# Optimization experiments

Hardware: AMD Instinct MI355X
Metric: run time of the kernel (lower is better)

Reference implementation:

```python
import jax, jax.numpy as jnp
import numpy as np

T, B = 128, 256          # frames, batch (free dims)
C_IN = 201               # in_features
KD = 3                   # keypoint_dimensionality
NK = C_IN // KD          # 67 keypoints = attention seq len
E = 8                    # d_pose_embed
H = 2                    # heads
DH = E // H              # head dim = 4
L = 12                   # encoder layers
FF = 2 * E               # 16
OUT = 128                # output_size
EPS = 1e-5


def setup_inputs() -> dict:
    key = jax.random.key(0)
    ks = jax.random.split(key, 12)
    s = 0.1
    return {
        "pose_clip": jax.random.normal(ks[0], (T, B, C_IN), jnp.float32),
        "embed_w": jax.random.normal(ks[1], (E, KD), jnp.float32) * s,
        "embed_b": jax.random.normal(ks[2], (E,), jnp.float32) * s,
        "in_proj_w": jax.random.normal(ks[3], (L, 3 * E, E), jnp.float32) * s,
        "in_proj_b": jax.random.normal(ks[4], (L, 3 * E), jnp.float32) * s,
        "attn_out_w": jax.random.normal(ks[5], (L, E, E), jnp.float32) * s,
        "attn_out_b": jax.random.normal(ks[6], (L, E), jnp.float32) * s,
        "ff1_w": jax.random.normal(ks[7], (L, FF, E), jnp.float32) * s,
        "ff1_b": jax.random.normal(ks[8], (L, FF), jnp.float32) * s,
        "ff2_w": jax.random.normal(ks[9], (L, E, FF), jnp.float32) * s,
        "ff2_b": jax.random.normal(ks[10], (L, E), jnp.float32) * s,
        "ln1_g": jnp.ones((L, E), jnp.float32),
        "ln1_b": jnp.zeros((L, E), jnp.float32),
        "ln2_g": jnp.ones((L, E), jnp.float32),
        "ln2_b": jnp.zeros((L, E), jnp.float32),
        "out_w": jax.random.normal(ks[11], (OUT, NK * E), jnp.float32) * s,
        "out_b": jnp.zeros((OUT,), jnp.float32),
    }


def _ln(x, g, b):
    m = jnp.mean(x, axis=-1, keepdims=True)
    v = jnp.mean(jnp.square(x - m), axis=-1, keepdims=True)
    return (x - m) * jax.lax.rsqrt(v + EPS) * g + b


def _encoder(x, layer_params):
    # x: [S, N, E]; post-LN TransformerEncoderLayer, relu activation, no dropout (eval)
    def step(h, p):
        ipw, ipb, aow, aob, f1w, f1b, f2w, f2b, g1, b1, g2, b2 = p
        S, N, _ = h.shape
        qkv = h @ ipw.T + ipb                      # [S, N, 3E]
        q, k, v = jnp.split(qkv, 3, axis=-1)
        q = q.reshape(S, N, H, DH)
        k = k.reshape(S, N, H, DH)
        v = v.reshape(S, N, H, DH)
        scores = jnp.einsum('snhd,tnhd->nhst', q, k) / np.sqrt(DH).astype(h.dtype)
        attn = jax.nn.softmax(scores, axis=-1)
        o = jnp.einsum('nhst,tnhd->snhd', attn, v).reshape(S, N, E)
        o = o @ aow.T + aob
        h = _ln(h + o, g1, b1)
        ff = jax.nn.relu(h @ f1w.T + f1b) @ f2w.T + f2b
        h = _ln(h + ff, g2, b2)
        return h, None
    x, _ = jax.lax.scan(step, x, layer_params)
    return x


def reference(pose_clip, embed_w, embed_b, in_proj_w, in_proj_b, attn_out_w,
              attn_out_b, ff1_w, ff1_b, ff2_w, ff2_b, ln1_g, ln1_b, ln2_g,
              ln2_b, out_w, out_b):
    t, b, c = pose_clip.shape
    nk = c // KD
    # [t,b,c] -> [t*b, nk, 3] -> [nk, t*b, 3]  (seq=keypoints, batch=t*b)
    x = pose_clip.reshape(t * b, nk, KD).transpose(1, 0, 2)
    x = x @ embed_w.T + embed_b                    # [nk, t*b, E]
    layer_params = (in_proj_w, in_proj_b, attn_out_w, attn_out_b,
                    ff1_w, ff1_b, ff2_w, ff2_b, ln1_g, ln1_b, ln2_g, ln2_b)
    x = _encoder(x, layer_params)
    x = x.transpose(1, 0, 2).reshape(t, b, nk * E)  # [t, b, 536]
    return jnp.tanh(x @ out_w.T + out_b)            # [t, b, 128]
```

## Files before the change

kernel.cpp:

```cpp
#include <hip/hip_runtime.h>
#include <math.h>

#define NTOT 32768
#define CIN  201
#define S    67
#define E    8
#define H    2
#define L    12
#define FF   16
#define OUTC 128
#define KF   536
#define EPB  7
#define LPE  34
#define THREADS 256
#define NPAIR 34

typedef float v2f __attribute__((ext_vector_type(2)));

#if __has_builtin(__builtin_amdgcn_exp2f)
#define EXP2F(x) __builtin_amdgcn_exp2f(x)
#else
#define EXP2F(x) exp2f(x)
#endif
#if __has_builtin(__builtin_amdgcn_rcpf)
#define RCPF(x) __builtin_amdgcn_rcpf(x)
#else
#define RCPF(x) (1.0f/(x))
#endif
#if __has_builtin(__builtin_amdgcn_rsqf)
#define RSQF(x) __builtin_amdgcn_rsqf(x)
#else
#define RSQF(x) rsqrtf(x)
#endif

#define QSCALE 0.7213475204444817f

__device__ __forceinline__ v2f sp(float x) { return (v2f){x, x}; }

__device__ __forceinline__ void ln8p(v2f* x, const float* __restrict__ gg,
                                     const float* __restrict__ bb) {
    v2f m = {0.f, 0.f};
    #pragma unroll
    for (int e = 0; e < E; ++e) m += x[e];
    m *= 0.125f;
    v2f v = {0.f, 0.f};
    #pragma unroll
    for (int e = 0; e < E; ++e) { v2f d = x[e] - m; v += d * d; }
    v *= 0.125f;
    v2f rs;
    rs.x = RSQF(v.x + 1e-5f);
    rs.y = RSQF(v.y + 1e-5f);
    #pragma unroll
    for (int e = 0; e < E; ++e) x[e] = (x[e] - m) * rs * sp(gg[e]) + sp(bb[e]);
}

__global__ __launch_bounds__(THREADS, 5)
void enc_kernel(const float* __restrict__ pose,
                const float* __restrict__ ew,  const float* __restrict__ ebias,
                const float* __restrict__ ipw, const float* __restrict__ ipb,
                const float* __restrict__ aow, const float* __restrict__ aob,
                const float* __restrict__ f1w, const float* __restrict__ f1b,
                const float* __restrict__ f2w, const float* __restrict__ f2b,
                const float* __restrict__ g1,  const float* __restrict__ b1,
                const float* __restrict__ g2,  const float* __restrict__ b2,
                float* __restrict__ xf)
{
    __shared__ float4 KA[EPB * H][NPAIR];
    __shared__ float4 KB[EPB * H][NPAIR];
    __shared__ float4 VA[EPB * H][NPAIR];
    __shared__ float4 VB[EPB * H][NPAIR];

    const int lid = threadIdx.x;
    const int g   = lid / LPE;
    const int j   = lid - g * LPE;
    const int n   = blockIdx.x * EPB + g;
    const bool active = (g < EPB) && (n < NTOT);
    const bool pad = (j == LPE - 1);
    const int r0 = 2 * j;

    v2f xr[E];
    if (active) {
        const float* p0 = pose + (size_t)n * CIN + 3 * r0;
        const float* p1 = pad ? p0 : (p0 + 3);
        v2f c0 = {p0[0], p1[0]};
        v2f c1 = {p0[1], p1[1]};
        v2f c2 = {p0[2], p1[2]};
        #pragma unroll
        for (int e = 0; e < E; ++e)
            xr[e] = sp(ebias[e]) + c0 * sp(ew[e*3+0]) + c1 * sp(ew[e*3+1])
                                 + c2 * sp(ew[e*3+2]);
    }

    #pragma unroll 1
    for (int l = 0; l < L; ++l) {
        const float* W  = ipw + l * 192;
        const float* Bq = ipb + l * 24;

        v2f qp[E];
        if (active) {
            v2f qkv[24];
            #pragma unroll
            for (int jo = 0; jo < 24; ++jo) {
                v2f a = sp(Bq[jo]);
                #pragma unroll
                for (int e = 0; e < E; ++e) a += xr[e] * sp(W[jo*8 + e]);
                qkv[jo] = a;
            }
            #pragma unroll
            for (int c = 0; c < E; ++c) qp[c] = qkv[c] * QSCALE;
            if (pad) {
                #pragma unroll
                for (int c = 8; c < 24; ++c) qkv[c].y = 0.f;
            }
            #pragma unroll
            for (int h = 0; h < H; ++h) {
                const int gh = g*2 + h;
                KA[gh][j] = make_float4(qkv[8+4*h+0].x, qkv[8+4*h+0].y,
                                        qkv[8+4*h+1].x, qkv[8+4*h+1].y);
                KB[gh][j] = make_float4(qkv[8+4*h+2].x, qkv[8+4*h+2].y,
                                        qkv[8+4*h+3].x, qkv[8+4*h+3].y);
                VA[gh][j] = make_float4(qkv[16+4*h+0].x, qkv[16+4*h+0].y,
                                        qkv[16+4*h+1].x, qkv[16+4*h+1].y);
                VB[gh][j] = make_float4(qkv[16+4*h+2].x, qkv[16+4*h+2].y,
                                        qkv[16+4*h+3].x, qkv[16+4*h+3].y);
            }
        }
        __syncthreads();

        if (active) {
            v2f os[E];
            #pragma unroll
            for (int h = 0; h < H; ++h) {
                const int gh = g*2 + h;
                const float4* pKA = KA[gh];
                const float4* pKB = KB[gh];
                const float4* pVA = VA[gh];
                const float4* pVB = VB[gh];
                const v2f q0l = sp(qp[4*h+0].x), q0h = sp(qp[4*h+0].y);
                const v2f q1l = sp(qp[4*h+1].x), q1h = sp(qp[4*h+1].y);
                const v2f q2l = sp(qp[4*h+2].x), q2h = sp(qp[4*h+2].y);
                const v2f q3l = sp(qp[4*h+3].x), q3h = sp(qp[4*h+3].y);
                v2f ls0 = {0.f,0.f}, ls1 = {0.f,0.f};
                v2f oc00={0.f,0.f}, oc01={0.f,0.f}, oc02={0.f,0.f}, oc03={0.f,0.f};
                v2f oc10={0.f,0.f}, oc11={0.f,0.f}, oc12={0.f,0.f}, oc13={0.f,0.f};
                #pragma unroll
                for (int i = 0; i < NPAIR; ++i) {
                    float4 ka = pKA[i], kb = pKB[i];
                    float4 va = pVA[i], vb = pVB[i];
                    v2f kx = *(const v2f*)&ka.x, ky = *(const v2f*)&ka.z;
                    v2f kz = *(const v2f*)&kb.x, kw = *(const v2f*)&kb.z;
                    v2f sc0 = q0l*kx + q1l*ky + q2l*kz + q3l*kw;
                    v2f sc1 = q0h*kx + q1h*ky + q2h*kz + q3h*kw;
                    v2f e0, e1;
                    e0.x = EXP2F(sc0.x);  e0.y = EXP2F(sc0.y);
                    e1.x = EXP2F(sc1.x);  e1.y = EXP2F(sc1.y);
                    ls0 += e0;  ls1 += e1;
                    v2f v0 = *(const v2f*)&va.x, v1 = *(const v2f*)&va.z;
                    v2f v2 = *(const v2f*)&vb.x, v3 = *(const v2f*)&vb.z;
                    oc00 += e0*v0; oc01 += e0*v1; oc02 += e0*v2; oc03 += e0*v3;
                    oc10 += e1*v0; oc11 += e1*v1; oc12 += e1*v2; oc13 += e1*v3;
                }
                float l0 = ls0.x + ls0.y - 1.0f;
                float l1 = ls1.x + ls1.y - 1.0f;
                float i0 = RCPF(l0), i1 = RCPF(l1);
                os[4*h+0] = (v2f){(oc00.x+oc00.y)*i0, (oc10.x+oc10.y)*i1};
                os[4*h+1] = (v2f){(oc01.x+oc01.y)*i0, (oc11.x+oc11.y)*i1};
                os[4*h+2] = (v2f){(oc02.x+oc02.y)*i0, (oc12.x+oc12.y)*i1};
                os[4*h+3] = (v2f){(oc03.x+oc03.y)*i0, (oc13.x+oc13.y)*i1};
            }

            {
                const float* WA = aow + l*64;
                const float* BA = aob + l*8;
                #pragma unroll
                for (int e = 0; e < E; ++e) {
                    v2f a = sp(BA[e]);
                    #pragma unroll
                    for (int e2 = 0; e2 < E; ++e2) a += os[e2] * sp(WA[e*8 + e2]);
                    xr[e] += a;
                }
            }
            ln8p(xr, g1 + l*E, b1 + l*E);

            {
                const float* W1 = f1w + l*128;
                const float* B1 = f1b + l*16;
                const float* W2 = f2w + l*128;
                const float* B2 = f2b + l*8;
                v2f t1[FF];
                #pragma unroll
                for (int f = 0; f < FF; ++f) {
                    v2f a = sp(B1[f]);
                    #pragma unroll
                    for (int e = 0; e < E; ++e) a += xr[e] * sp(W1[f*8 + e]);
                    a.x = fmaxf(a.x, 0.f);
                    a.y = fmaxf(a.y, 0.f);
                    t1[f] = a;
                }
                #pragma unroll
                for (int e = 0; e < E; ++e) {
                    v2f a = sp(B2[e]);
                    #pragma unroll
                    for (int f = 0; f < FF; ++f) a += t1[f] * sp(W2[e*16 + f]);
                    xr[e] += a;
                }
            }
            ln8p(xr, g2 + l*E, b2 + l*E);
        }
        __syncthreads();
    }

    if (active) {
        float* dst = xf + (size_t)n * KF + r0 * E;
        *(float4*)(dst + 0) = make_float4(xr[0].x, xr[1].x, xr[2].x, xr[3].x);
        *(float4*)(dst + 4) = make_float4(xr[4].x, xr[5].x, xr[6].x, xr[7].x);
        if (!pad) {
            *(float4*)(dst + 8)  = make_float4(xr[0].y, xr[1].y, xr[2].y, xr[3].y);
            *(float4*)(dst + 12) = make_float4(xr[4].y, xr[5].y, xr[6].y, xr[7].y);
        }
    }
}

__global__ void tr_kernel(const float* __restrict__ ow, float* __restrict__ wt)
{
    int i = blockIdx.x * 256 + threadIdx.x;
    if (i < OUTC * KF) {
        int c = i / KF, k = i - c * KF;
        wt[k * OUTC + c] = ow[i];
    }
}

__global__ __launch_bounds__(256, 4)
void out_kernel(const float* __restrict__ xf, const float* __restrict__ wt,
                const float* __restrict__ ob, float* __restrict__ out)
{
    __shared__ float Xs[32][68];
    const int lid = threadIdx.x;
    const int tx  = lid & 31;
    const int ty  = lid >> 5;
    const int n0  = blockIdx.x * 32;

    float acc[4][4] = {};

    #pragma unroll 1
    for (int kc = 0; kc < 9; ++kc) {
        const int kb = kc * 64;
        const int kw = (kc < 8) ? 64 : 24;
        __syncthreads();
        const int nvec = 32 * (kw >> 2);
        for (int i = lid; i < nvec; i += 256) {
            int r = i / (kw >> 2), kq = i - r * (kw >> 2);
            *(float4*)&Xs[r][kq*4] =
                *(const float4*)&xf[(size_t)(n0 + r) * KF + kb + kq*4];
        }
        __syncthreads();
        #pragma unroll 4
        for (int k = 0; k < kw; ++k) {
            float4 w4 = *(const float4*)&wt[(size_t)(kb + k) * OUTC + tx*4];
            #pragma unroll
            for (int i = 0; i < 4; ++i) {
                float x = Xs[ty*4 + i][k];
                acc[i][0] += x*w4.x; acc[i][1] += x*w4.y;
                acc[i][2] += x*w4.z; acc[i][3] += x*w4.w;
            }
        }
    }

    const float4 bb = *(const float4*)&ob[tx*4];
    #pragma unroll
    for (int i = 0; i < 4; ++i) {
        int r = n0 + ty*4 + i;
        float4 v;
        v.x = tanhf(acc[i][0] + bb.x);
        v.y = tanhf(acc[i][1] + bb.y);
        v.z = tanhf(acc[i][2] + bb.z);
        v.w = tanhf(acc[i][3] + bb.w);
        *(float4*)(out + (size_t)r * OUTC + tx*4) = v;
    }
}

extern "C" void kernel_launch(void* const* d_in, const int* in_sizes, int n_in,
                              void* d_out, int out_size, void* d_ws, size_t ws_size,
                              hipStream_t stream) {
    (void)in_sizes; (void)n_in; (void)out_size; (void)ws_size;
    const float* pose = (const float*)d_in[0];
    const float* ew   = (const float*)d_in[1];
    const float* eb   = (const float*)d_in[2];
    const float* ipw  = (const float*)d_in[3];
    const float* ipb  = (const float*)d_in[4];
    const float* aow  = (const float*)d_in[5];
    const float* aob  = (const float*)d_in[6];
    const float* f1w  = (const float*)d_in[7];
    const float* f1b  = (const float*)d_in[8];
    const float* f2w  = (const float*)d_in[9];
    const float* f2b  = (const float*)d_in[10];
    const float* g1   = (const float*)d_in[11];
    const float* b1   = (const float*)d_in[12];
    const float* g2   = (const float*)d_in[13];
    const float* b2   = (const float*)d_in[14];
    const float* ow   = (const float*)d_in[15];
    const float* ob   = (const float*)d_in[16];

    float* xf = (float*)d_ws;
    float* wt = xf + (size_t)NTOT * KF;

    const int grid1 = (NTOT + EPB - 1) / EPB;
    enc_kernel<<<grid1, THREADS, 0, stream>>>(pose, ew, eb, ipw, ipb, aow, aob,
                                              f1w, f1b, f2w, f2b, g1, b1, g2, b2, xf);
    tr_kernel<<<(OUTC*KF + 255)/256, 256, 0, stream>>>(ow, wt);
    out_kernel<<<NTOT / 32, 256, 0, stream>>>(xf, wt, ob, (float*)d_out);
}
```

Measured before the change: 1.355 ms.

## Store K/V as packed fp16 and use fdot2 in attention inner loop

Packs keys and values into half-precision pairs in shared memory, halving LDS storage and read traffic. The score and weighted-value accumulations switch from packed fp32 FMAs to v_dot2 fp16 instructions with fp32 accumulation, and exp weights are rounded to fp16. Q is now computed after the K/V store, and launch bounds rise to 8 blocks per CU for higher occupancy. This trades attention accuracy (fp16 rounding of scores, weights and values) for fewer instructions and less shared-memory pressure.

Result: no change. 1.372 ms (+1.3%).

```diff
diff --git a/kernel.cpp b/kernel.cpp
--- a/kernel.cpp
+++ b/kernel.cpp
@@ -16,6 +16,7 @@
 #define NPAIR 34
 
 typedef float v2f __attribute__((ext_vector_type(2)));
+typedef __fp16 h2  __attribute__((ext_vector_type(2)));
 
 #if __has_builtin(__builtin_amdgcn_exp2f)
 #define EXP2F(x) __builtin_amdgcn_exp2f(x)
@@ -31,6 +32,26 @@
 #define RSQF(x) __builtin_amdgcn_rsqf(x)
 #else
 #define RSQF(x) rsqrtf(x)
+#endif
+
+#if __has_builtin(__builtin_amdgcn_cvt_pkrtz)
+__device__ __forceinline__ h2 cvh(float a, float b) {
+    return __builtin_amdgcn_cvt_pkrtz(a, b);
+}
+#else
+__device__ __forceinline__ h2 cvh(float a, float b) {
+    h2 r; r.x = (__fp16)a; r.y = (__fp16)b; return r;
+}
+#endif
+__device__ __forceinline__ float pkf(float a, float b) {
+    return __builtin_bit_cast(float, cvh(a, b));
+}
+__device__ __forceinline__ h2 bch(float f) { return __builtin_bit_cast(h2, f); }
+
+#if __has_builtin(__builtin_amdgcn_fdot2)
+#define FDOT2(a, b, c) __builtin_amdgcn_fdot2((a), (b), (c), false)
+#else
+#define FDOT2(a, b, c) ((float)(a).x*(float)(b).x + (float)(a).y*(float)(b).y + (c))
 #endif
 
 #define QSCALE 0.7213475204444817f
@@ -54,7 +75,7 @@
     for (int e = 0; e < E; ++e) x[e] = (x[e] - m) * rs * sp(gg[e]) + sp(bb[e]);
 }
 
-__global__ __launch_bounds__(THREADS, 5)
+__global__ __launch_bounds__(THREADS, 8)
 void enc_kernel(const float* __restrict__ pose,
                 const float* __restrict__ ew,  const float* __restrict__ ebias,
                 const float* __restrict__ ipw, const float* __restrict__ ipb,
@@ -65,10 +86,8 @@
                 const float* __restrict__ g2,  const float* __restrict__ b2,
                 float* __restrict__ xf)
 {
-    __shared__ float4 KA[EPB * H][NPAIR];
-    __shared__ float4 KB[EPB * H][NPAIR];
-    __shared__ float4 VA[EPB * H][NPAIR];
-    __shared__ float4 VB[EPB * H][NPAIR];
+    __shared__ float4 Kh[EPB * H][NPAIR];
+    __shared__ float4 Vh[EPB * H][NPAIR];
 
     const int lid = threadIdx.x;
     const int g   = lid / LPE;
@@ -96,77 +115,95 @@
         const float* W  = ipw + l * 192;
         const float* Bq = ipb + l * 24;
 
-        v2f qp[E];
+        h2 qh[8];
         if (active) {
-            v2f qkv[24];
-            #pragma unroll
-            for (int jo = 0; jo < 24; ++jo) {
-                v2f a = sp(Bq[jo]);
-                #pragma unroll
-                for (int e = 0; e < E; ++e) a += xr[e] * sp(W[jo*8 + e]);
-                qkv[jo] = a;
-            }
-            #pragma unroll
-            for (int c = 0; c < E; ++c) qp[c] = qkv[c] * QSCALE;
+            v2f kv[16];
+            #pragma unroll
+            for (int jo = 0; jo < 16; ++jo) {
+                v2f a = sp(Bq[8 + jo]);
+                #pragma unroll
+                for (int e = 0; e < E; ++e) a += xr[e] * sp(W[(8+jo)*8 + e]);
+                kv[jo] = a;
+            }
             if (pad) {
                 #pragma unroll
-                for (int c = 8; c < 24; ++c) qkv[c].y = 0.f;
+                for (int c = 0; c < 16; ++c) kv[c].y = 0.f;
             }
             #pragma unroll
             for (int h = 0; h < H; ++h) {
                 const int gh = g*2 + h;
-                KA[gh][j] = make_float4(qkv[8+4*h+0].x, qkv[8+4*h+0].y,
-                                        qkv[8+4*h+1].x, qkv[8+4*h+1].y);
-                KB[gh][j] = make_float4(qkv[8+4*h+2].x, qkv[8+4*h+2].y,
-                                        qkv[8+4*h+3].x, qkv[8+4*h+3].y);
-                VA[gh][j] = make_float4(qkv[16+4*h+0].x, qkv[16+4*h+0].y,
-                                        qkv[16+4*h+1].x, qkv[16+4*h+1].y);
-                VB[gh][j] = make_float4(qkv[16+4*h+2].x, qkv[16+4*h+2].y,
-                                        qkv[16+4*h+3].x, qkv[16+4*h+3].y);
+                Kh[gh][j] = make_float4(
+                    pkf(kv[4*h+0].x, kv[4*h+1].x),
+                    pkf(kv[4*h+2].x, kv[4*h+3].x),
+                    pkf(kv[4*h+0].y, kv[4*h+1].y),
+                    pkf(kv[4*h+2].y, kv[4*h+3].y));
+                Vh[gh][j] = make_float4(
+                    pkf(kv[8+4*h+0].x, kv[8+4*h+0].y),
+                    pkf(kv[8+4*h+1].x, kv[8+4*h+1].y),
+                    pkf(kv[8+4*h+2].x, kv[8+4*h+2].y),
+                    pkf(kv[8+4*h+3].x, kv[8+4*h+3].y));
+            }
+            #pragma unroll
+            for (int h = 0; h < H; ++h) {
+                v2f q[4];
+                #pragma unroll
+                for (int c = 0; c < 4; ++c) {
+                    v2f a = sp(Bq[4*h + c]);
+                    #pragma unroll
+                    for (int e = 0; e < E; ++e) a += xr[e] * sp(W[(4*h+c)*8 + e]);
+                    q[c] = a * QSCALE;
+                }
+                qh[4*h+0] = cvh(q[0].x, q[1].x);
+                qh[4*h+1] = cvh(q[2].x, q[3].x);
+                qh[4*h+2] = cvh(q[0].y, q[1].y);
+                qh[4*h+3] = cvh(q[2].y, q[3].y);
             }
         }
         __syncthreads();
 
         if (active) {
+            const h2 one2 = cvh(1.0f, 1.0f);
             v2f os[E];
             #pragma unroll
             for (int h = 0; h < H; ++h) {
                 const int gh = g*2 + h;
-                const float4* pKA = KA[gh];
-                const float4* pKB = KB[gh];
-                const float4* pVA = VA[gh];
-                const float4* pVB = VB[gh];
-                const v2f q0l = sp(qp[4*h+0].x), q0h = sp(qp[4*h+0].y);
-                const v2f q1l = sp(qp[4*h+1].x), q1h = sp(qp[4*h+1].y);
-                const v2f q2l = sp(qp[4*h+2].x), q2h = sp(qp[4*h+2].y);
-                const v2f q3l = sp(qp[4*h+3].x), q3h = sp(qp[4*h+3].y);
-                v2f ls0 = {0.f,0.f}, ls1 = {0.f,0.f};
-                v2f oc00={0.f,0.f}, oc01={0.f,0.f}, oc02={0.f,0.f}, oc03={0.f,0.f};
-                v2f oc10={0.f,0.f}, oc11={0.f,0.f}, oc12={0.f,0.f}, oc13={0.f,0.f};
+                const float4* pK = Kh[gh];
+                const float4* pV = Vh[gh];
+                const h2 q01_0 = qh[4*h+0], q23_0 = qh[4*h+1];
+                const h2 q01_1 = qh[4*h+2], q23_1 = qh[4*h+3];
+                float ls0 = 0.f, ls1 = 0.f;
+                float oc00=0.f, oc01=0.f, oc02=0.f, oc03=0.f;
+                float oc10=0.f, oc11=0.f, oc12=0.f, oc13=0.f;
                 #pragma unroll
                 for (int i = 0; i < NPAIR; ++i) {
-                    float4 ka = pKA[i], kb = pKB[i];
-                    float4 va = pVA[i], vb = pVB[i];
-                    v2f kx = *(const v2f*)&ka.x, ky = *(const v2f*)&ka.z;
-                    v2f kz = *(const v2f*)&kb.x, kw = *(const v2f*)&kb.z;
-                    v2f sc0 = q0l*kx + q1l*ky + q2l*kz + q3l*kw;
-                    v2f sc1 = q0h*kx + q1h*ky + q2h*kz + q3h*kw;
-                    v2f e0, e1;
-                    e0.x = EXP2F(sc0.x);  e0.y = EXP2F(sc0.y);
-                    e1.x = EXP2F(sc1.x);  e1.y = EXP2F(sc1.y);
-                    ls0 += e0;  ls1 += e1;
-                    v2f v0 = *(const v2f*)&va.x, v1 = *(const v2f*)&va.z;
-                    v2f v2 = *(const v2f*)&vb.x, v3 = *(const v2f*)&vb.z;
-                    oc00 += e0*v0; oc01 += e0*v1; oc02 += e0*v2; oc03 += e0*v3;
-                    oc10 += e1*v0; oc11 += e1*v1; oc12 += e1*v2; oc13 += e1*v3;
-                }
-                float l0 = ls0.x + ls0.y - 1.0f;
-                float l1 = ls1.x + ls1.y - 1.0f;
+                    float4 kk = pK[i];
+                    float4 vv = pV[i];
+                    h2 ka = bch(kk.x), kb = bch(kk.y);
+                    h2 kc = bch(kk.z), kd = bch(kk.w);
+                    float s00 = FDOT2(q01_0, ka, FDOT2(q23_0, kb, 0.f));
+                    float s01 = FDOT2(q01_0, kc, FDOT2(q23_0, kd, 0.f));
+                    float s10 = FDOT2(q01_1, ka, FDOT2(q23_1, kb, 0.f));
+                    float s11 = FDOT2(q01_1, kc, FDOT2(q23_1, kd, 0.f));
+                    float e00 = EXP2F(s00), e01 = EXP2F(s01);
+                    float e10 = EXP2F(s10), e11 = EXP2F(s11);
+                    h2 ep0 = cvh(e00, e01);
+                    h2 ep1 = cvh(e10, e11);
+                    ls0 = FDOT2(ep0, one2, ls0);
+                    ls1 = FDOT2(ep1, one2, ls1);
+                    h2 v0 = bch(vv.x), v1 = bch(vv.y);
+                    h2 v2 = bch(vv.z), v3 = bch(vv.w);
+                    oc00 = FDOT2(ep0, v0, oc00); oc01 = FDOT2(ep0, v1, oc01);
+                    oc02 = FDOT2(ep0, v2, oc02); oc03 = FDOT2(ep0, v3, oc03);
+                    oc10 = FDOT2(ep1, v0, oc10); oc11 = FDOT2(ep1, v1, oc11);
+                    oc12 = FDOT2(ep1, v2, oc12); oc13 = FDOT2(ep1, v3, oc13);
+                }
+                float l0 = ls0 - 1.0f;
+                float l1 = ls1 - 1.0f;
                 float i0 = RCPF(l0), i1 = RCPF(l1);
-                os[4*h+0] = (v2f){(oc00.x+oc00.y)*i0, (oc10.x+oc10.y)*i1};
-                os[4*h+1] = (v2f){(oc01.x+oc01.y)*i0, (oc11.x+oc11.y)*i1};
-                os[4*h+2] = (v2f){(oc02.x+oc02.y)*i0, (oc12.x+oc12.y)*i1};
-                os[4*h+3] = (v2f){(oc03.x+oc03.y)*i0, (oc13.x+oc13.y)*i1};
+                os[4*h+0] = (v2f){oc00*i0, oc10*i1};
+                os[4*h+1] = (v2f){oc01*i0, oc11*i1};
+                os[4*h+2] = (v2f){oc02*i0, oc12*i1};
+                os[4*h+3] = (v2f){oc03*i0, oc13*i1};
             }
 
             {
```

## Process attention heads sequentially to halve LDS and raise occupancy

Applied to the files above, without the earlier changes.

Computes the QKV projection one head at a time, so each head's K/V is staged in LDS buffers half the previous size and fewer registers stay live. The launch bound rises from 5 to 8 waves per SIMD. The aim is more resident waves to hide latency. In exchange the kernel runs four block barriers per layer instead of two, and the tighter register budget may cause spills.

Result: slower. 1.815 ms (+33.9%).

```diff
diff --git a/kernel.cpp b/kernel.cpp
--- a/kernel.cpp
+++ b/kernel.cpp
@@ -54,7 +54,7 @@
     for (int e = 0; e < E; ++e) x[e] = (x[e] - m) * rs * sp(gg[e]) + sp(bb[e]);
 }
 
-__global__ __launch_bounds__(THREADS, 5)
+__global__ __launch_bounds__(THREADS, 8)
 void enc_kernel(const float* __restrict__ pose,
                 const float* __restrict__ ew,  const float* __restrict__ ebias,
                 const float* __restrict__ ipw, const float* __restrict__ ipb,
@@ -65,10 +65,10 @@
                 const float* __restrict__ g2,  const float* __restrict__ b2,
                 float* __restrict__ xf)
 {
-    __shared__ float4 KA[EPB * H][NPAIR];
-    __shared__ float4 KB[EPB * H][NPAIR];
-    __shared__ float4 VA[EPB * H][NPAIR];
-    __shared__ float4 VB[EPB * H][NPAIR];
+    __shared__ float4 KA[EPB][NPAIR];
+    __shared__ float4 KB[EPB][NPAIR];
+    __shared__ float4 VA[EPB][NPAIR];
+    __shared__ float4 VB[EPB][NPAIR];
 
     const int lid = threadIdx.x;
     const int g   = lid / LPE;
@@ -96,50 +96,45 @@
         const float* W  = ipw + l * 192;
         const float* Bq = ipb + l * 24;
 
-        v2f qp[E];
-        if (active) {
-            v2f qkv[24];
-            #pragma unroll
-            for (int jo = 0; jo < 24; ++jo) {
-                v2f a = sp(Bq[jo]);
-                #pragma unroll
-                for (int e = 0; e < E; ++e) a += xr[e] * sp(W[jo*8 + e]);
-                qkv[jo] = a;
-            }
-            #pragma unroll
-            for (int c = 0; c < E; ++c) qp[c] = qkv[c] * QSCALE;
-            if (pad) {
-                #pragma unroll
-                for (int c = 8; c < 24; ++c) qkv[c].y = 0.f;
-            }
-            #pragma unroll
-            for (int h = 0; h < H; ++h) {
-                const int gh = g*2 + h;
-                KA[gh][j] = make_float4(qkv[8+4*h+0].x, qkv[8+4*h+0].y,
-                                        qkv[8+4*h+1].x, qkv[8+4*h+1].y);
-                KB[gh][j] = make_float4(qkv[8+4*h+2].x, qkv[8+4*h+2].y,
-                                        qkv[8+4*h+3].x, qkv[8+4*h+3].y);
-                VA[gh][j] = make_float4(qkv[16+4*h+0].x, qkv[16+4*h+0].y,
-                                        qkv[16+4*h+1].x, qkv[16+4*h+1].y);
-                VB[gh][j] = make_float4(qkv[16+4*h+2].x, qkv[16+4*h+2].y,
-                                        qkv[16+4*h+3].x, qkv[16+4*h+3].y);
-            }
-        }
-        __syncthreads();
-
-        if (active) {
-            v2f os[E];
-            #pragma unroll
-            for (int h = 0; h < H; ++h) {
-                const int gh = g*2 + h;
-                const float4* pKA = KA[gh];
-                const float4* pKB = KB[gh];
-                const float4* pVA = VA[gh];
-                const float4* pVB = VB[gh];
-                const v2f q0l = sp(qp[4*h+0].x), q0h = sp(qp[4*h+0].y);
-                const v2f q1l = sp(qp[4*h+1].x), q1h = sp(qp[4*h+1].y);
-                const v2f q2l = sp(qp[4*h+2].x), q2h = sp(qp[4*h+2].y);
-                const v2f q3l = sp(qp[4*h+3].x), q3h = sp(qp[4*h+3].y);
+        v2f os[E];
+
+        #pragma unroll
+        for (int h = 0; h < H; ++h) {
+            v2f qp[4];
+            v2f kvp[8];
+            if (active) {
+                #pragma unroll
+                for (int c = 0; c < 12; ++c) {
+                    const int jo = 4*h + c + ((c >> 2) << 2);
+                    v2f a = sp(Bq[jo]);
+                    #pragma unroll
+                    for (int e = 0; e < E; ++e) a += xr[e] * sp(W[jo*8 + e]);
+                    if (c < 4) qp[c] = a * QSCALE;
+                    else       kvp[c-4] = a;
+                }
+                if (pad) {
+                    #pragma unroll
+                    for (int c = 0; c < 8; ++c) kvp[c].y = 0.f;
+                }
+            }
+            __syncthreads();
+            if (active) {
+                KA[g][j] = make_float4(kvp[0].x, kvp[0].y, kvp[1].x, kvp[1].y);
+                KB[g][j] = make_float4(kvp[2].x, kvp[2].y, kvp[3].x, kvp[3].y);
+                VA[g][j] = make_float4(kvp[4].x, kvp[4].y, kvp[5].x, kvp[5].y);
+                VB[g][j] = make_float4(kvp[6].x, kvp[6].y, kvp[7].x, kvp[7].y);
+            }
+            __syncthreads();
+
+            if (active) {
+                const float4* pKA = KA[g];
+                const float4* pKB = KB[g];
+                const float4* pVA = VA[g];
+                const float4* pVB = VB[g];
+                const v2f q0l = sp(qp[0].x), q0h = sp(qp[0].y);
+                const v2f q1l = sp(qp[1].x), q1h = sp(qp[1].y);
+                const v2f q2l = sp(qp[2].x), q2h = sp(qp[2].y);
+                const v2f q3l = sp(qp[3].x), q3h = sp(qp[3].y);
                 v2f ls0 = {0.f,0.f}, ls1 = {0.f,0.f};
                 v2f oc00={0.f,0.f}, oc01={0.f,0.f}, oc02={0.f,0.f}, oc03={0.f,0.f};
                 v2f oc10={0.f,0.f}, oc11={0.f,0.f}, oc12={0.f,0.f}, oc13={0.f,0.f};
@@ -168,7 +163,9 @@
                 os[4*h+2] = (v2f){(oc02.x+oc02.y)*i0, (oc12.x+oc12.y)*i1};
                 os[4*h+3] = (v2f){(oc03.x+oc03.y)*i0, (oc13.x+oc13.y)*i1};
             }
-
+        }
+
+        if (active) {
             {
                 const float* WA = aow + l*64;
                 const float* BA = aob + l*8;
@@ -207,7 +204,6 @@
             }
             ln8p(xr, g2 + l*E, b2 + l*E);
         }
-        __syncthreads();
     }
 
     if (active) {
```
